# Optimization experiments

Measured on AMD Instinct MI355X. Metric: run time of the kernel, lower is better.

Reference implementation:

```python
import jax, jax.numpy as jnp
import numpy as np


def _spectral_norm(W, u):
    # W: [out, in] (1x1 conv weight flattened), u: [out]
    # one power-iteration step (torch does this under no_grad), then
    # sigma = u' @ W @ v with gradient flowing through W only.
    v = W.T @ u
    v = v / jnp.linalg.norm(v)
    u2 = W @ v
    u2 = u2 / jnp.linalg.norm(u2)
    v = jax.lax.stop_gradient(v)
    u2 = jax.lax.stop_gradient(u2)
    sigma = u2 @ (W @ v)
    return W / sigma


def setup_inputs() -> dict:
    key = jax.random.key(0)
    ks = jax.random.split(key, 8)
    B, C, H, W = 32, 512, 32, 32
    Cq = C // 8  # 64
    x = jax.random.normal(ks[0], (B, C, H, W), dtype=jnp.float32)
    s = 1.0 / np.sqrt(C)
    return {
        "x": x,
        "Wq": jax.random.normal(ks[1], (Cq, C), dtype=jnp.float32) * s,
        "bq": jnp.zeros((Cq,), dtype=jnp.float32),
        "uq": jax.random.normal(ks[2], (Cq,), dtype=jnp.float32),
        "Wk": jax.random.normal(ks[3], (Cq, C), dtype=jnp.float32) * s,
        "bk": jnp.zeros((Cq,), dtype=jnp.float32),
        "uk": jax.random.normal(ks[4], (Cq,), dtype=jnp.float32),
        "Wv": jax.random.normal(ks[5], (C, C), dtype=jnp.float32) * s,
        "bv": jnp.zeros((C,), dtype=jnp.float32),
        "uv": jax.random.normal(ks[6], (C,), dtype=jnp.float32),
        "gamma": jnp.float32(0.5),
    }


def reference(x, Wq, bq, uq, Wk, bk, uk, Wv, bv, uv, gamma):
    B, C, H, W = x.shape
    N = H * W
    f = x.reshape(B, C, N)                                   # [B,C,N]
    # 1x1 conv == channel matmul with spectral-normalized weights
    q = jnp.einsum('oc,bcn->bno', _spectral_norm(Wq, uq), f) + bq          # [B,N,Cq]
    k = jnp.einsum('oc,bcn->bon', _spectral_norm(Wk, uk), f) + bk[:, None]  # [B,Cq,N]
    v = jnp.einsum('oc,bcn->bon', _spectral_norm(Wv, uv), f) + bv[:, None]  # [B,C,N]
    qk = jnp.einsum('bno,bom->bnm', q, k)                    # [B,N,N], no 1/sqrt(d)
    attn = jax.nn.softmax(qk, axis=1)                        # softmax over QUERY axis (dim 1)
    o = jnp.einsum('bcn,bnm->bcm', v, attn).reshape(B, C, H, W)
    return gamma * o + x
```

## Files before the change

kernel.cpp:

```cpp
#include <hip/hip_runtime.h>
#include <hip/hip_bf16.h>

typedef __hip_bfloat16 bf16;
typedef __bf16 bf16x8 __attribute__((ext_vector_type(8)));
typedef float  f32x4  __attribute__((ext_vector_type(4)));
typedef unsigned short u16x8 __attribute__((ext_vector_type(8)));

#define C_IN  512
#define N_SP  1024
#define BATCH 32

__device__ __forceinline__ float ldmix(const void* p, size_t i, int f32) {
    return f32 ? ((const float*)p)[i] : __bfloat162float(((const bf16*)p)[i]);
}
__device__ __forceinline__ void stmix(void* p, size_t i, float v, int f32) {
    if (f32) ((float*)p)[i] = v;
    else     ((bf16*)p)[i] = __float2bfloat16(v);
}
__device__ __forceinline__ unsigned short bfbits(float f) {
    bf16 t = __float2bfloat16(f);
    return *reinterpret_cast<unsigned short*>(&t);
}
__device__ __forceinline__ float bf2f(unsigned short h) {
    union { unsigned u; float f; } c; c.u = ((unsigned)h) << 16; return c.f;
}
__device__ __forceinline__ void ldvec8(const void* W, size_t base, int f32, float v[8]) {
    if (f32) {
        const float4* p = reinterpret_cast<const float4*>((const float*)W + base);
        float4 a = p[0], b = p[1];
        v[0] = a.x; v[1] = a.y; v[2] = a.z; v[3] = a.w;
        v[4] = b.x; v[5] = b.y; v[6] = b.z; v[7] = b.w;
    } else {
        u16x8 h = *reinterpret_cast<const u16x8*>((const bf16*)W + base);
#pragma unroll
        for (int j = 0; j < 8; ++j) v[j] = bf2f(h[j]);
    }
}

__device__ __forceinline__ void gload_lds16(const bf16* g, void* l) {
    __builtin_amdgcn_global_load_lds(
        (__attribute__((address_space(1))) void*)(g),
        (__attribute__((address_space(3))) void*)(l),
        16, 0, 0);
}

#define STAGE128(LDS, GROW, GPITCH, K0) do {                                   \
    int _c = (wave << 7) + lane; int _r = _c >> 2;                             \
    int _s = (_c & 3) ^ ((_r >> 1) & 3);                                       \
    gload_lds16((GROW) + (size_t)_r * (GPITCH) + (K0) + _s * 8,                \
                (char*)(LDS) + (wave << 11));                                  \
    _c += 64; _r = _c >> 2; _s = (_c & 3) ^ ((_r >> 1) & 3);                   \
    gload_lds16((GROW) + (size_t)_r * (GPITCH) + (K0) + _s * 8,                \
                (char*)(LDS) + (wave << 11) + 1024);                           \
} while (0)

#define STAGE64(LDS, GROW, GPITCH, K0) do {                                    \
    int _c = (wave << 6) + lane; int _r = _c >> 2;                             \
    int _s = (_c & 3) ^ ((_r >> 1) & 3);                                       \
    gload_lds16((GROW) + (size_t)_r * (GPITCH) + (K0) + _s * 8,                \
                (char*)(LDS) + (wave << 10));                                  \
} while (0)

__device__ __forceinline__ bf16x8 swz_frag(const void* tile, int row, int quad) {
    return *(const bf16x8*)((const char*)tile + (row << 6) +
                            ((quad ^ ((row >> 1) & 3)) << 4));
}

__device__ __forceinline__ void tile_decode(int bid, int nblk, int& z, int& mc) {
    int GBk = nblk >> 5;
    if ((GBk & 7) == 0) {
        z  = (bid & 7) + 8 * ((bid >> 3) >> 5);
        mc = (bid >> 3) & 31;
    } else {
        z  = bid >> 5;
        mc = bid & 31;
    }
}

__global__ void k_detect(const unsigned short* __restrict__ xh, int* __restrict__ flag)
{
    __shared__ int red[256];
    int tid = threadIdx.x;
    unsigned short h = xh[2 * tid];
    int e = (h >> 7) & 0xFF;
    red[tid] = (e == 0 || (e >= 96 && e <= 159)) ? 1 : 0;
    __syncthreads();
    for (int s = 128; s > 0; s >>= 1) { if (tid < s) red[tid] += red[tid + s]; __syncthreads(); }
    if (tid == 0) *flag = (red[0] < 192) ? 1 : 0;
}

__global__ __launch_bounds__(256) void k_sn1(
    const void* __restrict__ Wq, const void* __restrict__ uq,
    const void* __restrict__ Wk, const void* __restrict__ uk,
    const void* __restrict__ Wv, const void* __restrict__ uv,
    const int* __restrict__ flag, float* __restrict__ tpart)
{
    __shared__ float sh_u[64];
    __shared__ float sh_acc[4][512];
    int f32 = *flag;
    int bx = blockIdx.x;
    const void *W, *u; int oc, slot;
    if (bx == 0)      { W = Wq; u = uq; oc = 0;      slot = 0; }
    else if (bx == 1) { W = Wk; u = uk; oc = 0;      slot = 1; }
    else              { W = Wv; u = uv; oc = bx - 2; slot = bx; }
    int tid = threadIdx.x, wave = tid >> 6, lane = tid & 63;
    if (tid < 64) sh_u[tid] = ldmix(u, oc * 64 + tid, f32);
    __syncthreads();

    float acc[8];
#pragma unroll
    for (int j = 0; j < 8; ++j) acc[j] = 0.f;
    int obase = oc * 64 + wave * 16;
#pragma unroll 4
    for (int i = 0; i < 16; ++i) {
        int o = obase + i;
        float w8[8]; ldvec8(W, (size_t)o * C_IN + lane * 8, f32, w8);
        float uo = sh_u[o - oc * 64];
#pragma unroll
        for (int j = 0; j < 8; ++j) acc[j] += w8[j] * uo;
    }
#pragma unroll
    for (int j = 0; j < 8; ++j) sh_acc[wave][lane * 8 + j] = acc[j];
    __syncthreads();
    for (int c = tid; c < 512; c += 256)
        tpart[(size_t)slot * 512 + c] =
            sh_acc[0][c] + sh_acc[1][c] + sh_acc[2][c] + sh_acc[3][c];
}

__global__ __launch_bounds__(512) void k_sn2(
    const void* __restrict__ Wq, const void* __restrict__ Wk,
    const void* __restrict__ Wv, const int* __restrict__ flag,
    const float* __restrict__ tpart, float* __restrict__ sig)
{
    __shared__ float sh_t[512];
    __shared__ float red[512];
    int f32 = *flag;
    int m = blockIdx.x;
    const void* W; int out, slot0, nch;
    if (m == 0)      { W = Wq; out = 64;  slot0 = 0; nch = 1; }
    else if (m == 1) { W = Wk; out = 64;  slot0 = 1; nch = 1; }
    else             { W = Wv; out = 512; slot0 = 2; nch = 8; }
    int tid = threadIdx.x, wave = tid >> 6, lane = tid & 63;

    float t = 0.f;
    for (int c2 = 0; c2 < nch; ++c2) t += tpart[(size_t)(slot0 + c2) * 512 + tid];
    sh_t[tid] = t;
    red[tid] = t * t;
    __syncthreads();
    for (int s = 256; s > 0; s >>= 1) { if (tid < s) red[tid] += red[tid + s]; __syncthreads(); }
    float t2 = red[0];
    __syncthreads();

    float tl[8];
#pragma unroll
    for (int j = 0; j < 8; ++j) tl[j] = sh_t[lane * 8 + j];

    float s2 = 0.f;
#pragma unroll 2
    for (int o = wave; o < out; o += 8) {
        float w8[8]; ldvec8(W, (size_t)o * C_IN + lane * 8, f32, w8);
        float d = 0.f;
#pragma unroll
        for (int j = 0; j < 8; ++j) d += w8[j] * tl[j];
#pragma unroll
        for (int off = 32; off > 0; off >>= 1) d += __shfl_xor(d, off);
        if (lane == 0) s2 += d * d;
    }
    __syncthreads();
    red[tid] = (lane == 0) ? s2 : 0.f;
    __syncthreads();
    for (int s = 256; s > 0; s >>= 1) { if (tid < s) red[tid] += red[tid + s]; __syncthreads(); }
    if (tid == 0) sig[m] = sqrtf(t2 / red[0]);
}

__global__ __launch_bounds__(256) void k_wscale(
    const void* __restrict__ Wq, const void* __restrict__ bq,
    const void* __restrict__ Wk, const void* __restrict__ bk,
    const void* __restrict__ Wv, const void* __restrict__ bv,
    const float* __restrict__ sig, const int* __restrict__ flag,
    bf16* __restrict__ Wb, bf16* __restrict__ Wlo, float* __restrict__ biasf)
{
    int f32 = *flag;
    int r = blockIdx.x;
    const void *W, *b; int row; float s;
    if (r < 64)       { W = Wq; b = bq; row = r;       s = sig[0]; }
    else if (r < 128) { W = Wk; b = bk; row = r - 64;  s = sig[1]; }
    else              { W = Wv; b = bv; row = r - 128; s = sig[2]; }
    for (int c = threadIdx.x; c < C_IN; c += 256) {
        float w = ldmix(W, (size_t)row * C_IN + c, f32) * s;
        bf16 hi = __float2bfloat16(w);
        Wb[(size_t)r * C_IN + c] = hi;
        if (r < 128)
            Wlo[(size_t)r * C_IN + c] = __float2bfloat16(w - __bfloat162float(hi));
    }
    if (threadIdx.x == 0) biasf[r] = ldmix(b, row, f32);
}

__global__ __launch_bounds__(256) void k_xt(
    const void* __restrict__ x, const int* __restrict__ flag,
    char* __restrict__ SX, int batch0)
{
    __shared__ float tile[64][65];
    int f32 = *flag;
    int z = blockIdx.z;
    int n0 = blockIdx.x * 64, c0 = blockIdx.y * 64;
    size_t xoff = (size_t)(batch0 + z) * C_IN * N_SP;
    bf16* xTh = (bf16*)(SX + (size_t)z * 4194304);
    bf16* xTl = xTh + 524288;
    int tid = threadIdx.x;
#pragma unroll
    for (int i = 0; i < 4; ++i) {
        int idx = tid + i * 256;
        int c = idx >> 4, nq = idx & 15;
#pragma unroll
        for (int t = 0; t < 4; ++t)
            tile[c][nq * 4 + t] = ldmix(x, xoff + (size_t)(c0 + c) * N_SP + n0 + nq * 4 + t, f32);
    }
    __syncthreads();
#pragma unroll
    for (int i = 0; i < 16; ++i) {
        int idx = tid + i * 256;
        int n = idx >> 6, c = idx & 63;
        float v = tile[c][n];
        bf16 hi = __float2bfloat16(v);
        xTh[(size_t)(n0 + n) * C_IN + c0 + c] = hi;
        xTl[(size_t)(n0 + n) * C_IN + c0 + c] = __float2bfloat16(v - __bfloat162float(hi));
    }
}

__global__ __launch_bounds__(256) void k_qkv_v(
    const bf16* __restrict__ Wb, const float* __restrict__ biasf,
    const char* __restrict__ SX, bf16* __restrict__ YV)
{
    __shared__ __bf16 As0[128][32], As1[128][32], As2[128][32];
    __shared__ __bf16 Bs0[128][32], Bs1[128][32], Bs2[128][32];
    int z, mc; tile_decode(blockIdx.x, gridDim.x, z, mc);
    int n0 = (mc >> 2) * 128;
    int r0 = 128 + (mc & 3) * 128;
    const bf16* xTh = (const bf16*)(SX + (size_t)z * 4194304);
    bf16* Yv = YV + (size_t)z * 524288;
    int tid = threadIdx.x, wave = tid >> 6, lane = tid & 63, quad = lane >> 4, l16 = lane & 15;
    int wc = (wave >> 1) * 64, wm = (wave & 1) * 64;

    const bf16* Ar = Wb + (size_t)r0 * C_IN;
    const bf16* Br = xTh + (size_t)n0 * C_IN;

    f32x4 acc[4][4];
#pragma unroll
    for (int i = 0; i < 4; ++i)
#pragma unroll
        for (int j = 0; j < 4; ++j) acc[i][j] = (f32x4){0.f, 0.f, 0.f, 0.f};

    STAGE128(As0, Ar, C_IN, 0);  STAGE128(Bs0, Br, C_IN, 0);
    STAGE128(As1, Ar, C_IN, 32); STAGE128(Bs1, Br, C_IN, 32);
    char *a0 = (char*)As0, *a1 = (char*)As1, *a2 = (char*)As2;
    char *b0 = (char*)Bs0, *b1 = (char*)Bs1, *b2 = (char*)Bs2;

#define QKV_V_MFMA(PA, PB) {                                                   \
    bf16x8 a[4], b[4];                                                         \
    _Pragma("unroll")                                                          \
    for (int i = 0; i < 4; ++i) a[i] = swz_frag(PA, wc + i * 16 + l16, quad);  \
    _Pragma("unroll")                                                          \
    for (int j = 0; j < 4; ++j) b[j] = swz_frag(PB, wm + j * 16 + l16, quad);  \
    __builtin_amdgcn_s_setprio(1);                                             \
    _Pragma("unroll")                                                          \
    for (int i = 0; i < 4; ++i)                                                \
        _Pragma("unroll")                                                      \
        for (int j = 0; j < 4; ++j)                                            \
            acc[i][j] = __builtin_amdgcn_mfma_f32_16x16x32_bf16(a[i], b[j], acc[i][j], 0, 0, 0); \
    __builtin_amdgcn_s_setprio(0); }

    for (int t = 0; t < 15; ++t) {
        asm volatile("s_waitcnt vmcnt(4)" ::: "memory");
        __builtin_amdgcn_s_barrier();
        __builtin_amdgcn_sched_barrier(0);
        if (t + 2 < 16) {
            int k2 = (t + 2) * 32;
            STAGE128(a2, Ar, C_IN, k2); STAGE128(b2, Br, C_IN, k2);
        }
        QKV_V_MFMA(a0, b0);
        char* tp = a0; a0 = a1; a1 = a2; a2 = tp;
        tp = b0; b0 = b1; b1 = b2; b2 = tp;
    }
    asm volatile("s_waitcnt vmcnt(0)" ::: "memory");
    __builtin_amdgcn_s_barrier();
    __builtin_amdgcn_sched_barrier(0);
    QKV_V_MFMA(a0, b0);
#undef QKV_V_MFMA

#pragma unroll
    for (int i = 0; i < 4; ++i)
#pragma unroll
        for (int j = 0; j < 4; ++j)
#pragma unroll
            for (int r = 0; r < 4; ++r) {
                int c = r0 + wc + i * 16 + quad * 4 + r;
                int n = n0 + wm + j * 16 + l16;
                Yv[(size_t)(c - 128) * N_SP + n] = __float2bfloat16(acc[i][j][r] + biasf[c]);
            }
}

__global__ __launch_bounds__(256) void k_qkv_qk(
    const bf16* __restrict__ Wb, const bf16* __restrict__ Wlo,
    const float* __restrict__ biasf, const char* __restrict__ SX,
    bf16* __restrict__ QT, bf16* __restrict__ KT)
{
    __shared__ __bf16 Ah_[3][64][32], Al_[3][64][32], Bh_[3][64][32], Bl_[3][64][32];
    int z, mc; tile_decode(blockIdx.x, gridDim.x, z, mc);
    int n0 = (mc >> 1) * 64;
    int m0 = (mc & 1) * 64;
    const bf16* xTh = (const bf16*)(SX + (size_t)z * 4194304);
    const bf16* xTl = xTh + 524288;
    bf16* qt = QT + (size_t)z * 65536;
    bf16* kt = KT + (size_t)z * 65536;
    int tid = threadIdx.x, wave = tid >> 6, lane = tid & 63, quad = lane >> 4, l16 = lane & 15;
    int wmh = (wave >> 1) * 32, wnh = (wave & 1) * 32;

    const bf16* Ahr = Wb  + (size_t)m0 * C_IN;
    const bf16* Alr = Wlo + (size_t)m0 * C_IN;
    const bf16* Bhr = xTh + (size_t)n0 * C_IN;
    const bf16* Blr = xTl + (size_t)n0 * C_IN;

    f32x4 acc[2][2];
#pragma unroll
    for (int i = 0; i < 2; ++i)
#pragma unroll
        for (int j = 0; j < 2; ++j) acc[i][j] = (f32x4){0.f, 0.f, 0.f, 0.f};

    STAGE64(Ah_[0], Ahr, C_IN, 0);  STAGE64(Al_[0], Alr, C_IN, 0);
    STAGE64(Bh_[0], Bhr, C_IN, 0);  STAGE64(Bl_[0], Blr, C_IN, 0);
    STAGE64(Ah_[1], Ahr, C_IN, 32); STAGE64(Al_[1], Alr, C_IN, 32);
    STAGE64(Bh_[1], Bhr, C_IN, 32); STAGE64(Bl_[1], Blr, C_IN, 32);
    char *ah0 = (char*)Ah_[0], *ah1 = (char*)Ah_[1], *ah2 = (char*)Ah_[2];
    char *al0 = (char*)Al_[0], *al1 = (char*)Al_[1], *al2 = (char*)Al_[2];
    char *bh0 = (char*)Bh_[0], *bh1 = (char*)Bh_[1], *bh2 = (char*)Bh_[2];
    char *bl0 = (char*)Bl_[0], *bl1 = (char*)Bl_[1], *bl2 = (char*)Bl_[2];

#define QK_MFMA(PAH, PAL, PBH, PBL) {                                          \
    bf16x8 fah[2], fal[2], fbh[2], fbl[2];                                     \
    _Pragma("unroll")                                                          \
    for (int i = 0; i < 2; ++i) {                                              \
        fah[i] = swz_frag(PAH, wmh + i * 16 + l16, quad);                      \
        fal[i] = swz_frag(PAL, wmh + i * 16 + l16, quad);                      \
    }                                                                          \
    _Pragma("unroll")                                                          \
    for (int j = 0; j < 2; ++j) {                                              \
        fbh[j] = swz_frag(PBH, wnh + j * 16 + l16, quad);                      \
        fbl[j] = swz_frag(PBL, wnh + j * 16 + l16, quad);                      \
    }                                                                          \
    __builtin_amdgcn_s_setprio(1);                                             \
    _Pragma("unroll")                                                          \
    for (int i = 0; i < 2; ++i)                                                \
        _Pragma("unroll")                                                      \
        for (int j = 0; j < 2; ++j) {                                          \
            acc[i][j] = __builtin_amdgcn_mfma_f32_16x16x32_bf16(fah[i], fbh[j], acc[i][j], 0, 0, 0); \
            acc[i][j] = __builtin_amdgcn_mfma_f32_16x16x32_bf16(fah[i], fbl[j], acc[i][j], 0, 0, 0); \
            acc[i][j] = __builtin_amdgcn_mfma_f32_16x16x32_bf16(fal[i], fbh[j], acc[i][j], 0, 0, 0); \
        }                                                                      \
    __builtin_amdgcn_s_setprio(0); }

    for (int t = 0; t < 15; ++t) {
        asm volatile("s_waitcnt vmcnt(4)" ::: "memory");
        __builtin_amdgcn_s_barrier();
        __builtin_amdgcn_sched_barrier(0);
        if (t + 2 < 16) {
            int k2 = (t + 2) * 32;
            STAGE64(ah2, Ahr, C_IN, k2); STAGE64(al2, Alr, C_IN, k2);
            STAGE64(bh2, Bhr, C_IN, k2); STAGE64(bl2, Blr, C_IN, k2);
        }
        QK_MFMA(ah0, al0, bh0, bl0);
        char* tp = ah0; ah0 = ah1; ah1 = ah2; ah2 = tp;
        tp = al0; al0 = al1; al1 = al2; al2 = tp;
        tp = bh0; bh0 = bh1; bh1 = bh2; bh2 = tp;
        tp = bl0; bl0 = bl1; bl1 = bl2; bl2 = tp;
    }
    asm volatile("s_waitcnt vmcnt(0)" ::: "memory");
    __builtin_amdgcn_s_barrier();
    __builtin_amdgcn_sched_barrier(0);
    QK_MFMA(ah0, al0, bh0, bl0);
#undef QK_MFMA

#pragma unroll
    for (int i = 0; i < 2; ++i)
#pragma unroll
        for (int j = 0; j < 2; ++j) {
            int cbase = m0 + wmh + i * 16 + quad * 4;
            int n = n0 + wnh + j * 16 + l16;
            ushort4 st;
            st.x = bfbits(acc[i][j][0] + biasf[cbase + 0]);
            st.y = bfbits(acc[i][j][1] + biasf[cbase + 1]);
            st.z = bfbits(acc[i][j][2] + biasf[cbase + 2]);
            st.w = bfbits(acc[i][j][3] + biasf[cbase + 3]);
            bf16* dst = (m0 == 0) ? &qt[(size_t)n * 64 + cbase]
                                  : &kt[(size_t)n * 64 + (cbase - 64)];
            *reinterpret_cast<ushort4*>(dst) = st;
        }
}

__global__ __launch_bounds__(256) void k_qk(
    const bf16* __restrict__ QT, const bf16* __restrict__ KT,
    char* __restrict__ SX)
{
    __shared__ __bf16 Als[128][40];
    __shared__ __bf16 Bls[128][40];
    int z = blockIdx.z, m0 = blockIdx.y * 128, n0 = blockIdx.x * 128;
    const bf16* qt = QT + (size_t)z * 65536;
    const bf16* kt = KT + (size_t)z * 65536;
    float* Sf = (float*)(SX + (size_t)z * 4194304);
    int tid = threadIdx.x, wave = tid >> 6, lane = tid & 63, quad = lane >> 4, l16 = lane & 15;
    int wc = (wave >> 1) * 64, wm = (wave & 1) * 64;

    f32x4 acc[4][4];
#pragma unroll
    for (int i = 0; i < 4; ++i)
#pragma unroll
        for (int j = 0; j < 4; ++j) acc[i][j] = (f32x4){0.f, 0.f, 0.f, 0.f};

#pragma unroll
    for (int k0 = 0; k0 < 64; k0 += 32) {
#pragma unroll
        for (int s = 0; s < 2; ++s) {
            int idx = tid + s * 256; int row = idx >> 2, ch = idx & 3;
            *reinterpret_cast<uint4*>(&Als[row][ch * 8]) =
                *reinterpret_cast<const uint4*>(&kt[(size_t)(m0 + row) * 64 + k0 + ch * 8]);
            *reinterpret_cast<uint4*>(&Bls[row][ch * 8]) =
                *reinterpret_cast<const uint4*>(&qt[(size_t)(n0 + row) * 64 + k0 + ch * 8]);
        }
        __syncthreads();
        bf16x8 a[4], b[4];
#pragma unroll
        for (int i = 0; i < 4; ++i)
            a[i] = *reinterpret_cast<const bf16x8*>(&Als[wc + i * 16 + l16][quad * 8]);
#pragma unroll
        for (int j = 0; j < 4; ++j)
            b[j] = *reinterpret_cast<const bf16x8*>(&Bls[wm + j * 16 + l16][quad * 8]);
#pragma unroll
        for (int i = 0; i < 4; ++i)
#pragma unroll
            for (int j = 0; j < 4; ++j)
                acc[i][j] = __builtin_amdgcn_mfma_f32_16x16x32_bf16(a[i], b[j], acc[i][j], 0, 0, 0);
        __syncthreads();
    }
#pragma unroll
    for (int i = 0; i < 4; ++i)
#pragma unroll
        for (int j = 0; j < 4; ++j)
#pragma unroll
            for (int r = 0; r < 4; ++r) {
                int m = m0 + wc + i * 16 + quad * 4 + r;
                int n = n0 + wm + j * 16 + l16;
                Sf[(size_t)m * N_SP + n] = acc[i][j][r];
            }
}

__global__ __launch_bounds__(256) void k_softmax(char* __restrict__ SX)
{
    __shared__ float red[256];
    int z = blockIdx.x >> 10, m = blockIdx.x & 1023;
    float* p = (float*)(SX + (size_t)z * 4194304) + (size_t)m * N_SP;
    bf16* pb = (bf16*)p;
    int tid = threadIdx.x;
    float v0 = p[tid], v1 = p[tid + 256], v2 = p[tid + 512], v3 = p[tid + 768];
    red[tid] = fmaxf(fmaxf(v0, v1), fmaxf(v2, v3));
    __syncthreads();
    for (int s = 128; s > 0; s >>= 1) { if (tid < s) red[tid] = fmaxf(red[tid], red[tid + s]); __syncthreads(); }
    float mx = red[0];
    __syncthreads();
    float d0 = fmaxf(fminf(v0 - mx, 0.f), -80.f);
    float d1 = fmaxf(fminf(v1 - mx, 0.f), -80.f);
    float d2 = fmaxf(fminf(v2 - mx, 0.f), -80.f);
    float d3 = fmaxf(fminf(v3 - mx, 0.f), -80.f);
    float e0 = __expf(d0), e1 = __expf(d1), e2 = __expf(d2), e3 = __expf(d3);
    red[tid] = e0 + e1 + e2 + e3;
    __syncthreads();
    for (int s = 128; s > 0; s >>= 1) { if (tid < s) red[tid] += red[tid + s]; __syncthreads(); }
    float inv = 1.f / red[0];
    pb[tid]       = __float2bfloat16(e0 * inv);
    pb[tid + 256] = __float2bfloat16(e1 * inv);
    pb[tid + 512] = __float2bfloat16(e2 * inv);
    pb[tid + 768] = __float2bfloat16(e3 * inv);
}

__global__ __launch_bounds__(256) void k_out(
    const bf16* __restrict__ YV, const char* __restrict__ SX,
    const void* __restrict__ x, const void* __restrict__ gamma,
    const int* __restrict__ flag, void* __restrict__ out, int batch0)
{
    __shared__ __bf16 As0[128][32], As1[128][32], As2[128][32];
    __shared__ __bf16 Bs0[128][32], Bs1[128][32], Bs2[128][32];
    int f32 = *flag;
    int z, mc; tile_decode(blockIdx.x, gridDim.x, z, mc);
    int m0 = (mc >> 2) * 128, c0 = (mc & 3) * 128;
    const bf16* Yv = YV + (size_t)z * 524288;
    const bf16* Pb = (const bf16*)(SX + (size_t)z * 4194304);
    int tid = threadIdx.x, wave = tid >> 6, lane = tid & 63, quad = lane >> 4, l16 = lane & 15;
    int wc = (wave >> 1) * 64, wm = (wave & 1) * 64;

    const bf16* Ar = Yv + (size_t)c0 * N_SP;
    const bf16* Br = Pb + (size_t)m0 * 2048;

    f32x4 acc[4][4];
#pragma unroll
    for (int i = 0; i < 4; ++i)
#pragma unroll
        for (int j = 0; j < 4; ++j) acc[i][j] = (f32x4){0.f, 0.f, 0.f, 0.f};

    STAGE128(As0, Ar, N_SP, 0);  STAGE128(Bs0, Br, 2048, 0);
    STAGE128(As1, Ar, N_SP, 32); STAGE128(Bs1, Br, 2048, 32);
    char *a0 = (char*)As0, *a1 = (char*)As1, *a2 = (char*)As2;
    char *b0 = (char*)Bs0, *b1 = (char*)Bs1, *b2 = (char*)Bs2;

#define OUT_MFMA(PA, PB) {                                                     \
    bf16x8 a[4], b[4];                                                         \
    _Pragma("unroll")                                                          \
    for (int i = 0; i < 4; ++i) a[i] = swz_frag(PA, wc + i * 16 + l16, quad);  \
    _Pragma("unroll")                                                          \
    for (int j = 0; j < 4; ++j) b[j] = swz_frag(PB, wm + j * 16 + l16, quad);  \
    __builtin_amdgcn_s_setprio(1);                                             \
    _Pragma("unroll")                                                          \
    for (int i = 0; i < 4; ++i)                                                \
        _Pragma("unroll")                                                      \
        for (int j = 0; j < 4; ++j)                                            \
            acc[i][j] = __builtin_amdgcn_mfma_f32_16x16x32_bf16(a[i], b[j], acc[i][j], 0, 0, 0); \
    __builtin_amdgcn_s_setprio(0); }

    for (int t = 0; t < 31; ++t) {
        asm volatile("s_waitcnt vmcnt(4)" ::: "memory");
        __builtin_amdgcn_s_barrier();
        __builtin_amdgcn_sched_barrier(0);
        if (t + 2 < 32) {
            int k2 = (t + 2) * 32;
            STAGE128(a2, Ar, N_SP, k2); STAGE128(b2, Br, 2048, k2);
        }
        OUT_MFMA(a0, b0);
        char* tp = a0; a0 = a1; a1 = a2; a2 = tp;
        tp = b0; b0 = b1; b1 = b2; b2 = tp;
    }
    asm volatile("s_waitcnt vmcnt(0)" ::: "memory");
    __builtin_amdgcn_s_barrier();
    __builtin_amdgcn_sched_barrier(0);
    OUT_MFMA(a0, b0);
#undef OUT_MFMA

    float g = ldmix(gamma, 0, f32);
    const size_t base = (size_t)(batch0 + z) * C_IN * N_SP;
#pragma unroll
    for (int i = 0; i < 4; ++i)
#pragma unroll
        for (int j = 0; j < 4; ++j)
#pragma unroll
            for (int r = 0; r < 4; ++r) {
                int c = c0 + wc + i * 16 + quad * 4 + r;
                int m = m0 + wm + j * 16 + l16;
                size_t o = base + (size_t)c * N_SP + m;
                float v = fmaf(g, acc[i][j][r], ldmix(x, o, f32));
                if (!(v == v)) v = 5555.0f + 1000.0f * f32;
                stmix(out, o, v, f32);
            }
}

__global__ void k_wsfail(float* __restrict__ out, int n)
{
    int i = blockIdx.x * 256 + threadIdx.x;
    if (i < n) out[i] = 7777.0f;
}

extern "C" void kernel_launch(void* const* d_in, const int* in_sizes, int n_in,
                              void* d_out, int out_size, void* d_ws, size_t ws_size,
                              hipStream_t stream)
{
    const void* x  = d_in[0];
    const void* Wq = d_in[1];
    const void* bq = d_in[2];
    const void* Wk = d_in[4];
    const void* bk = d_in[5];
    const void* Wv = d_in[7];
    const void* bv = d_in[8];
    const void* uq = d_in[3];
    const void* uk = d_in[6];
    const void* uv = d_in[9];
    const void* gm = d_in[10];

    const size_t HDR = 790528;
    const size_t per = 4194304 + 131072 + 131072 + 1048576;
    int GB = 0;
    for (int g = 32; g >= 1; g >>= 1)
        if (HDR + (size_t)g * per <= ws_size) { GB = g; break; }
    if (GB == 0) {
        k_wsfail<<<(out_size + 255) / 256, 256, 0, stream>>>((float*)d_out, out_size);
        return;
    }
    char* ws = (char*)d_ws;
    int*   flag  = (int*)ws;
    float* sig   = (float*)(ws + 16);
    float* biasf = (float*)(ws + 256);
    bf16*  Wb    = (bf16*)(ws + 4096);
    bf16*  Wlo   = (bf16*)(ws + 659456);
    char*  SX    = ws + HDR;
    bf16*  QT    = (bf16*)(SX + (size_t)GB * 4194304);
    bf16*  KT    = QT + (size_t)GB * 65536;
    bf16*  YV    = KT + (size_t)GB * 65536;
    float* tpart = (float*)SX;

    k_detect<<<1, 256, 0, stream>>>((const unsigned short*)x, flag);
    k_sn1<<<10, 256, 0, stream>>>(Wq, uq, Wk, uk, Wv, uv, flag, tpart);
    k_sn2<<<3, 512, 0, stream>>>(Wq, Wk, Wv, flag, tpart, sig);
    k_wscale<<<640, 256, 0, stream>>>(Wq, bq, Wk, bk, Wv, bv, sig, flag, Wb, Wlo, biasf);
    for (int b0 = 0; b0 < BATCH; b0 += GB) {
        k_xt     <<<dim3(16, 8, GB), 256, 0, stream>>>(x, flag, SX, b0);
        k_qkv_v  <<<GB * 32, 256, 0, stream>>>(Wb, biasf, SX, YV);
        k_qkv_qk <<<GB * 32, 256, 0, stream>>>(Wb, Wlo, biasf, SX, QT, KT);
        k_qk     <<<dim3(8, 8, GB), 256, 0, stream>>>(QT, KT, SX);
        k_softmax<<<GB * 1024, 256, 0, stream>>>(SX);
        k_out    <<<GB * 32, 256, 0, stream>>>(YV, SX, x, gm, flag, d_out, b0);
    }
}
```

Before: 417.3 us.

## Enlarge V-projection and output GEMM tiles to 256x256 with 512-thread blocks

Rewrites the V-projection and output GEMM kernels to compute 256x256 output tiles with 8 waves. Each wave holds a 128x64 accumulator, and the K step is 64 with a 128B-row XOR swizzle, double-buffered in 128KB of dynamic LDS. The aim is more data reuse per load and fewer k-loop barriers. In exchange the grid shrinks fourfold, to GB*8 blocks at one block per CU, which may leave many of the 256 CUs idle. The pipeline also drops from three stages to two, which risks exposing load latency.

```diff
diff --git a/kernel.cpp b/kernel.cpp
--- a/kernel.cpp
+++ b/kernel.cpp
@@ -44,16 +44,6 @@
         16, 0, 0);
 }
 
-#define STAGE128(LDS, GROW, GPITCH, K0) do {                                   \
-    int _c = (wave << 7) + lane; int _r = _c >> 2;                             \
-    int _s = (_c & 3) ^ ((_r >> 1) & 3);                                       \
-    gload_lds16((GROW) + (size_t)_r * (GPITCH) + (K0) + _s * 8,                \
-                (char*)(LDS) + (wave << 11));                                  \
-    _c += 64; _r = _c >> 2; _s = (_c & 3) ^ ((_r >> 1) & 3);                   \
-    gload_lds16((GROW) + (size_t)_r * (GPITCH) + (K0) + _s * 8,                \
-                (char*)(LDS) + (wave << 11) + 1024);                           \
-} while (0)
-
 #define STAGE64(LDS, GROW, GPITCH, K0) do {                                    \
     int _c = (wave << 6) + lane; int _r = _c >> 2;                             \
     int _s = (_c & 3) ^ ((_r >> 1) & 3);                                       \
@@ -64,6 +54,22 @@
 __device__ __forceinline__ bf16x8 swz_frag(const void* tile, int row, int quad) {
     return *(const bf16x8*)((const char*)tile + (row << 6) +
                             ((quad ^ ((row >> 1) & 3)) << 4));
+}
+
+#define STG256(LBASE, GROW, GPITCH, K0) do {                                   \
+    _Pragma("unroll")                                                          \
+    for (int _i = 0; _i < 4; ++_i) {                                           \
+        int _c = ((wave * 4 + _i) << 6) + lane;                                \
+        int _r = _c >> 3;                                                      \
+        int _lc = (_c & 7) ^ (_r & 7);                                         \
+        gload_lds16((GROW) + (size_t)_r * (GPITCH) + (K0) + _lc * 8,           \
+                    (char*)(LBASE) + ((wave * 4 + _i) << 10));                 \
+    }                                                                          \
+} while (0)
+
+__device__ __forceinline__ bf16x8 frag64(const void* tile, int row, int c8) {
+    return *(const bf16x8*)((const char*)tile + (row << 7) +
+                            ((c8 ^ (row & 7)) << 4));
 }
 
 __device__ __forceinline__ void tile_decode(int bid, int nblk, int& z, int& mc) {
@@ -74,6 +80,16 @@
     } else {
         z  = bid >> 5;
         mc = bid & 31;
+    }
+}
+__device__ __forceinline__ void tile_decode8(int bid, int nblk, int& z, int& mc) {
+    int GBk = nblk >> 3;
+    if ((GBk & 7) == 0) {
+        z  = (bid & 7) + 8 * (bid >> 6);
+        mc = (bid >> 3) & 7;
+    } else {
+        z  = bid >> 3;
+        mc = bid & 7;
     }
 }
 
@@ -228,75 +244,73 @@
     }
 }
 
-__global__ __launch_bounds__(256) void k_qkv_v(
+__global__ __launch_bounds__(512, 1) void k_qkv_v(
     const bf16* __restrict__ Wb, const float* __restrict__ biasf,
     const char* __restrict__ SX, bf16* __restrict__ YV)
 {
-    __shared__ __bf16 As0[128][32], As1[128][32], As2[128][32];
-    __shared__ __bf16 Bs0[128][32], Bs1[128][32], Bs2[128][32];
-    int z, mc; tile_decode(blockIdx.x, gridDim.x, z, mc);
-    int n0 = (mc >> 2) * 128;
-    int r0 = 128 + (mc & 3) * 128;
+    extern __shared__ char lds[];
+    int z, mc; tile_decode8(blockIdx.x, gridDim.x, z, mc);
+    int r0 = 128 + (mc >> 2) * 256;
+    int n0 = (mc & 3) * 256;
     const bf16* xTh = (const bf16*)(SX + (size_t)z * 4194304);
     bf16* Yv = YV + (size_t)z * 524288;
     int tid = threadIdx.x, wave = tid >> 6, lane = tid & 63, quad = lane >> 4, l16 = lane & 15;
-    int wc = (wave >> 1) * 64, wm = (wave & 1) * 64;
+    int wr = wave >> 2, wc4 = wave & 3;
 
     const bf16* Ar = Wb + (size_t)r0 * C_IN;
     const bf16* Br = xTh + (size_t)n0 * C_IN;
 
-    f32x4 acc[4][4];
-#pragma unroll
-    for (int i = 0; i < 4; ++i)
+    f32x4 acc[8][4];
+#pragma unroll
+    for (int i = 0; i < 8; ++i)
 #pragma unroll
         for (int j = 0; j < 4; ++j) acc[i][j] = (f32x4){0.f, 0.f, 0.f, 0.f};
 
-    STAGE128(As0, Ar, C_IN, 0);  STAGE128(Bs0, Br, C_IN, 0);
-    STAGE128(As1, Ar, C_IN, 32); STAGE128(Bs1, Br, C_IN, 32);
-    char *a0 = (char*)As0, *a1 = (char*)As1, *a2 = (char*)As2;
-    char *b0 = (char*)Bs0, *b1 = (char*)Bs1, *b2 = (char*)Bs2;
-
-#define QKV_V_MFMA(PA, PB) {                                                   \
-    bf16x8 a[4], b[4];                                                         \
-    _Pragma("unroll")                                                          \
-    for (int i = 0; i < 4; ++i) a[i] = swz_frag(PA, wc + i * 16 + l16, quad);  \
-    _Pragma("unroll")                                                          \
-    for (int j = 0; j < 4; ++j) b[j] = swz_frag(PB, wm + j * 16 + l16, quad);  \
-    __builtin_amdgcn_s_setprio(1);                                             \
-    _Pragma("unroll")                                                          \
-    for (int i = 0; i < 4; ++i)                                                \
-        _Pragma("unroll")                                                      \
-        for (int j = 0; j < 4; ++j)                                            \
-            acc[i][j] = __builtin_amdgcn_mfma_f32_16x16x32_bf16(a[i], b[j], acc[i][j], 0, 0, 0); \
-    __builtin_amdgcn_s_setprio(0); }
-
-    for (int t = 0; t < 15; ++t) {
-        asm volatile("s_waitcnt vmcnt(4)" ::: "memory");
-        __builtin_amdgcn_s_barrier();
-        __builtin_amdgcn_sched_barrier(0);
-        if (t + 2 < 16) {
-            int k2 = (t + 2) * 32;
-            STAGE128(a2, Ar, C_IN, k2); STAGE128(b2, Br, C_IN, k2);
-        }
-        QKV_V_MFMA(a0, b0);
-        char* tp = a0; a0 = a1; a1 = a2; a2 = tp;
-        tp = b0; b0 = b1; b1 = b2; b2 = tp;
-    }
+    STG256(lds, Ar, C_IN, 0);
+    STG256(lds + 32768, Br, C_IN, 0);
     asm volatile("s_waitcnt vmcnt(0)" ::: "memory");
     __builtin_amdgcn_s_barrier();
     __builtin_amdgcn_sched_barrier(0);
-    QKV_V_MFMA(a0, b0);
-#undef QKV_V_MFMA
-
-#pragma unroll
-    for (int i = 0; i < 4; ++i)
-#pragma unroll
-        for (int j = 0; j < 4; ++j)
+
+    for (int t = 0; t < 8; ++t) {
+        const char* Ac = lds + (t & 1) * 65536;
+        const char* Bc = Ac + 32768;
+        if (t + 1 < 8) {
+            char* An = lds + ((t + 1) & 1) * 65536;
+            STG256(An, Ar, C_IN, (t + 1) * 64);
+            STG256(An + 32768, Br, C_IN, (t + 1) * 64);
+        }
+#pragma unroll
+        for (int kh = 0; kh < 2; ++kh) {
+            bf16x8 af[8], bfr[4];
+#pragma unroll
+            for (int fm = 0; fm < 8; ++fm)
+                af[fm] = frag64(Ac, wr * 128 + fm * 16 + l16, kh * 4 + quad);
+#pragma unroll
+            for (int fn = 0; fn < 4; ++fn)
+                bfr[fn] = frag64(Bc, wc4 * 64 + fn * 16 + l16, kh * 4 + quad);
+            __builtin_amdgcn_s_setprio(1);
+#pragma unroll
+            for (int fm = 0; fm < 8; ++fm)
+#pragma unroll
+                for (int fn = 0; fn < 4; ++fn)
+                    acc[fm][fn] = __builtin_amdgcn_mfma_f32_16x16x32_bf16(af[fm], bfr[fn], acc[fm][fn], 0, 0, 0);
+            __builtin_amdgcn_s_setprio(0);
+        }
+        asm volatile("s_waitcnt vmcnt(0)" ::: "memory");
+        __builtin_amdgcn_s_barrier();
+        __builtin_amdgcn_sched_barrier(0);
+    }
+
+#pragma unroll
+    for (int fm = 0; fm < 8; ++fm)
+#pragma unroll
+        for (int fn = 0; fn < 4; ++fn)
 #pragma unroll
             for (int r = 0; r < 4; ++r) {
-                int c = r0 + wc + i * 16 + quad * 4 + r;
-                int n = n0 + wm + j * 16 + l16;
-                Yv[(size_t)(c - 128) * N_SP + n] = __float2bfloat16(acc[i][j][r] + biasf[c]);
+                int c = r0 + wr * 128 + fm * 16 + quad * 4 + r;
+                int n = n0 + wc4 * 64 + fn * 16 + l16;
+                Yv[(size_t)(c - 128) * N_SP + n] = __float2bfloat16(acc[fm][fn][r] + biasf[c]);
             }
 }
 
@@ -481,79 +495,78 @@
     pb[tid + 768] = __float2bfloat16(e3 * inv);
 }
 
-__global__ __launch_bounds__(256) void k_out(
+__global__ __launch_bounds__(512, 1) void k_out(
     const bf16* __restrict__ YV, const char* __restrict__ SX,
     const void* __restrict__ x, const void* __restrict__ gamma,
     const int* __restrict__ flag, void* __restrict__ out, int batch0)
 {
-    __shared__ __bf16 As0[128][32], As1[128][32], As2[128][32];
-    __shared__ __bf16 Bs0[128][32], Bs1[128][32], Bs2[128][32];
+    extern __shared__ char lds[];
     int f32 = *flag;
-    int z, mc; tile_decode(blockIdx.x, gridDim.x, z, mc);
-    int m0 = (mc >> 2) * 128, c0 = (mc & 3) * 128;
+    int z, mc; tile_decode8(blockIdx.x, gridDim.x, z, mc);
+    int c0 = (mc >> 2) * 256;
+    int m0 = (mc & 3) * 256;
     const bf16* Yv = YV + (size_t)z * 524288;
     const bf16* Pb = (const bf16*)(SX + (size_t)z * 4194304);
     int tid = threadIdx.x, wave = tid >> 6, lane = tid & 63, quad = lane >> 4, l16 = lane & 15;
-    int wc = (wave >> 1) * 64, wm = (wave & 1) * 64;
+    int wr = wave >> 2, wc4 = wave & 3;
 
     const bf16* Ar = Yv + (size_t)c0 * N_SP;
     const bf16* Br = Pb + (size_t)m0 * 2048;
 
-    f32x4 acc[4][4];
-#pragma unroll
-    for (int i = 0; i < 4; ++i)
+    f32x4 acc[8][4];
+#pragma unroll
+    for (int i = 0; i < 8; ++i)
 #pragma unroll
         for (int j = 0; j < 4; ++j) acc[i][j] = (f32x4){0.f, 0.f, 0.f, 0.f};
 
-    STAGE128(As0, Ar, N_SP, 0);  STAGE128(Bs0, Br, 2048, 0);
-    STAGE128(As1, Ar, N_SP, 32); STAGE128(Bs1, Br, 2048, 32);
-    char *a0 = (char*)As0, *a1 = (char*)As1, *a2 = (char*)As2;
-    char *b0 = (char*)Bs0, *b1 = (char*)Bs1, *b2 = (char*)Bs2;
-
-#define OUT_MFMA(PA, PB) {                                                     \
-    bf16x8 a[4], b[4];                                                         \
-    _Pragma("unroll")                                                          \
-    for (int i = 0; i < 4; ++i) a[i] = swz_frag(PA, wc + i * 16 + l16, quad);  \
-    _Pragma("unroll")                                                          \
-    for (int j = 0; j < 4; ++j) b[j] = swz_frag(PB, wm + j * 16 + l16, quad);  \
-    __builtin_amdgcn_s_setprio(1);                                             \
-    _Pragma("unroll")                                                          \
-    for (int i = 0; i < 4; ++i)                                                \
-        _Pragma("unroll")                                                      \
-        for (int j = 0; j < 4; ++j)                                            \
-            acc[i][j] = __builtin_amdgcn_mfma_f32_16x16x32_bf16(a[i], b[j], acc[i][j], 0, 0, 0); \
-    __builtin_amdgcn_s_setprio(0); }
-
-    for (int t = 0; t < 31; ++t) {
-        asm volatile("s_waitcnt vmcnt(4)" ::: "memory");
-        __builtin_amdgcn_s_barrier();
-        __builtin_amdgcn_sched_barrier(0);
-        if (t + 2 < 32) {
-            int k2 = (t + 2) * 32;
-            STAGE128(a2, Ar, N_SP, k2); STAGE128(b2, Br, 2048, k2);
-        }
-        OUT_MFMA(a0, b0);
-        char* tp = a0; a0 = a1; a1 = a2; a2 = tp;
-        tp = b0; b0 = b1; b1 = b2; b2 = tp;
-    }
+    STG256(lds, Ar, N_SP, 0);
+    STG256(lds + 32768, Br, 2048, 0);
     asm volatile("s_waitcnt vmcnt(0)" ::: "memory");
     __builtin_amdgcn_s_barrier();
     __builtin_amdgcn_sched_barrier(0);
-    OUT_MFMA(a0, b0);
-#undef OUT_MFMA
+
+    for (int t = 0; t < 16; ++t) {
+        const char* Ac = lds + (t & 1) * 65536;
+        const char* Bc = Ac + 32768;
+        if (t + 1 < 16) {
+            char* An = lds + ((t + 1) & 1) * 65536;
+            STG256(An, Ar, N_SP, (t + 1) * 64);
+            STG256(An + 32768, Br, 2048, (t + 1) * 64);
+        }
+#pragma unroll
+        for (int kh = 0; kh < 2; ++kh) {
+            bf16x8 af[8], bfr[4];
+#pragma unroll
+            for (int fm = 0; fm < 8; ++fm)
+                af[fm] = frag64(Ac, wr * 128 + fm * 16 + l16, kh * 4 + quad);
+#pragma unroll
+            for (int fn = 0; fn < 4; ++fn)
+                bfr[fn] = frag64(Bc, wc4 * 64 + fn * 16 + l16, kh * 4 + quad);
+            __builtin_amdgcn_s_setprio(1);
+#pragma unroll
+            for (int fm = 0; fm < 8; ++fm)
+#pragma unroll
+                for (int fn = 0; fn < 4; ++fn)
+                    acc[fm][fn] = __builtin_amdgcn_mfma_f32_16x16x32_bf16(af[fm], bfr[fn], acc[fm][fn], 0, 0, 0);
+            __builtin_amdgcn_s_setprio(0);
+        }
+        asm volatile("s_waitcnt vmcnt(0)" ::: "memory");
+        __builtin_amdgcn_s_barrier();
+        __builtin_amdgcn_sched_barrier(0);
+    }
 
     float g = ldmix(gamma, 0, f32);
     const size_t base = (size_t)(batch0 + z) * C_IN * N_SP;
 #pragma unroll
-    for (int i = 0; i < 4; ++i)
-#pragma unroll
-        for (int j = 0; j < 4; ++j)
+    for (int fm = 0; fm < 8; ++fm)
+#pragma unroll
+        for (int fn = 0; fn < 4; ++fn)
 #pragma unroll
             for (int r = 0; r < 4; ++r) {
-                int c = c0 + wc + i * 16 + quad * 4 + r;
-                int m = m0 + wm + j * 16 + l16;
+                int c = c0 + wr * 128 + fm * 16 + quad * 4 + r;
+                int m = m0 + wc4 * 64 + fn * 16 + l16;
                 size_t o = base + (size_t)c * N_SP + m;
-                float v = fmaf(g, acc[i][j][r], ldmix(x, o, f32));
+                float v = fmaf(g, acc[fm][fn][r], ldmix(x, o, f32));
                 if (!(v == v)) v = 5555.0f + 1000.0f * f32;
                 stmix(out, o, v, f32);
             }
@@ -581,6 +594,15 @@
     const void* uv = d_in[9];
     const void* gm = d_in[10];
 
+    static int lds_opt_done = 0;
+    if (!lds_opt_done) {
+        (void)hipFuncSetAttribute(reinterpret_cast<const void*>(k_qkv_v),
+                                  hipFuncAttributeMaxDynamicSharedMemorySize, 131072);
+        (void)hipFuncSetAttribute(reinterpret_cast<const void*>(k_out),
+                                  hipFuncAttributeMaxDynamicSharedMemorySize, 131072);
+        lds_opt_done = 1;
+    }
+
     const size_t HDR = 790528;
     const size_t per = 4194304 + 131072 + 131072 + 1048576;
     int GB = 0;
@@ -608,10 +630,10 @@
     k_wscale<<<640, 256, 0, stream>>>(Wq, bq, Wk, bk, Wv, bv, sig, flag, Wb, Wlo, biasf);
     for (int b0 = 0; b0 < BATCH; b0 += GB) {
         k_xt     <<<dim3(16, 8, GB), 256, 0, stream>>>(x, flag, SX, b0);
-        k_qkv_v  <<<GB * 32, 256, 0, stream>>>(Wb, biasf, SX, YV);
+        k_qkv_v  <<<GB * 8, 512, 131072, stream>>>(Wb, biasf, SX, YV);
         k_qkv_qk <<<GB * 32, 256, 0, stream>>>(Wb, Wlo, biasf, SX, QT, KT);
         k_qk     <<<dim3(8, 8, GB), 256, 0, stream>>>(QT, KT, SX);
         k_softmax<<<GB * 1024, 256, 0, stream>>>(SX);
-        k_out    <<<GB * 32, 256, 0, stream>>>(YV, SX, x, gm, flag, d_out, b0);
-    }
-}
+        k_out    <<<GB * 8, 512, 131072, stream>>>(YV, SX, x, gm, flag, d_out, b0);
+    }
+}
```

Result: faster. 393.3 us (-5.8%).
